# Optimization experiments

Hardware: AMD Instinct MI355X
Metric: run time of the kernel (lower is better)

## Reference

```python
import jax, jax.numpy as jnp
import numpy as np

N = 50000
E = 800000
IN_CH = 128
HID = 32
HEADS = 4
OUT_CH = 2
NEG_SLOPE = 0.2


def setup_inputs() -> dict:
    key = jax.random.key(0)
    ks = jax.random.split(key, 10)
    x = jax.random.normal(ks[0], (N, IN_CH), dtype=jnp.float32)
    edge_index = jax.random.randint(ks[1], (2, E), 0, N, dtype=jnp.int32)
    s1 = 1.0 / np.sqrt(IN_CH)
    s2 = 1.0 / np.sqrt(HEADS * HID)
    return {
        "x": x,
        "edge_index": edge_index,
        "W1": jax.random.normal(ks[2], (IN_CH, HEADS * HID), dtype=jnp.float32) * s1,
        "a_src1": jax.random.normal(ks[3], (HEADS, HID), dtype=jnp.float32) * s2,
        "a_dst1": jax.random.normal(ks[4], (HEADS, HID), dtype=jnp.float32) * s2,
        "b1": jnp.zeros((HEADS * HID,), dtype=jnp.float32),
        "W2": jax.random.normal(ks[5], (HEADS * HID, 1 * OUT_CH), dtype=jnp.float32) * s2,
        "a_src2": jax.random.normal(ks[6], (1, OUT_CH), dtype=jnp.float32),
        "a_dst2": jax.random.normal(ks[7], (1, OUT_CH), dtype=jnp.float32),
        "b2": jnp.zeros((OUT_CH,), dtype=jnp.float32),
    }


def gat_layer(x, edge_index, W, a_src, a_dst, bias, heads, out_ch, concat):
    # PyG GATConv: linear -> per-node attn terms -> per-edge LeakyReLU ->
    # softmax over incoming edges (self-loops added) -> scatter-add aggregate.
    n = x.shape[0]
    loop = jnp.arange(n, dtype=edge_index.dtype)
    src = jnp.concatenate([edge_index[0], loop])  # [E+N]
    dst = jnp.concatenate([edge_index[1], loop])
    h = (x @ W).reshape(n, heads, out_ch)                 # [N, H, C]
    a_s = jnp.einsum('nhc,hc->nh', h, a_src)              # [N, H]
    a_d = jnp.einsum('nhc,hc->nh', h, a_dst)
    e = jax.nn.leaky_relu(a_s[src] + a_d[dst], NEG_SLOPE)  # [E+N, H]
    m = jax.ops.segment_max(e, dst, num_segments=n)
    m = jax.lax.stop_gradient(jnp.where(jnp.isfinite(m), m, 0.0))
    p = jnp.exp(e - m[dst])
    denom = jax.ops.segment_sum(p, dst, num_segments=n)
    alpha = p / (denom[dst] + 1e-16)                       # softmax per dst node
    msg = h[src] * alpha[:, :, None]                       # [E+N, H, C]
    out = jax.ops.segment_sum(msg, dst, num_segments=n)    # [N, H, C]
    out = out.reshape(n, heads * out_ch) if concat else out.mean(axis=1)
    return out + bias


def reference(x, edge_index, W1, a_src1, a_dst1, b1, W2, a_src2, a_dst2, b2):
    h = gat_layer(x, edge_index, W1, a_src1, a_dst1, b1, HEADS, HID, True)
    h = jax.nn.relu(h)  # dropout is identity in eval mode
    o = gat_layer(h, edge_index, W2, a_src2, a_dst2, b2, 1, OUT_CH, False)
    return jax.nn.log_softmax(o, axis=1)
```

## Files before the change

kernel.cpp:

```cpp
#include <hip/hip_runtime.h>
#include <hip/hip_bf16.h>

#define NEG_SLOPE 0.2f
#define INV_LN2 1.44269504088896340736f
#define BSH   6
#define BUKSZ 64
#define MAXBUK 1024
#define CHUNK 2048
#define CAP   2048
#define CAPSH 11
#define XPAD  136

typedef __attribute__((ext_vector_type(8))) short bf16x8;
typedef __attribute__((ext_vector_type(4))) float f32x4;

__device__ __forceinline__ float exp2lrelu(float z) {
    return __builtin_amdgcn_exp2f(fmaxf(z, NEG_SLOPE * z));
}

__device__ __forceinline__ unsigned short f2bf(float f) {
    unsigned int u = __float_as_uint(f);
    u = (u + 0x7fffu + ((u >> 16) & 1u)) >> 16;
    return (unsigned short)u;
}

__device__ __forceinline__ float2 bfpair(unsigned int u) {
    float2 r;
    r.x = __uint_as_float(u << 16);
    r.y = __uint_as_float(u & 0xffff0000u);
    return r;
}

__global__ __launch_bounds__(256) void k0_prep(const float* __restrict__ W1,
                                               const float* __restrict__ a_src1,
                                               const float* __restrict__ a_dst1,
                                               unsigned short* __restrict__ w1t,
                                               int* __restrict__ gcur, int nbuk) {
    int g = blockIdx.x * 256 + threadIdx.x;
    if (g < nbuk) gcur[g] = 0;
    if (g < 128 * 128) {
        int k = g >> 7, nn = g & 127;
        w1t[nn * 128 + k] = f2bf(W1[g]);
    } else if (g < 128 * 128 + 1024) {
        int e = g - 128 * 128;
        int row8 = e >> 7;
        int k = e & 127;
        int h = row8 & 3;
        const float* av = (row8 < 4) ? a_src1 : a_dst1;
        float s = 0.f;
#pragma unroll
        for (int c = 0; c < 32; ++c)
            s += W1[k * 128 + h * 32 + c] * av[h * 32 + c];
        w1t[(128 + row8) * 128 + k] = f2bf(s * INV_LN2);
    } else if (g < 128 * 128 + 2048) {
        int e = g - (128 * 128 + 1024);
        w1t[(136 + (e >> 7)) * 128 + (e & 127)] = 0;
    }
}

__global__ __launch_bounds__(256) void k1_fat(const float* __restrict__ x,
                                              const unsigned short* __restrict__ w1t,
                                              unsigned short* __restrict__ h1b,
                                              float* __restrict__ a_s1,
                                              float* __restrict__ a_d1, int n,
                                              const int* __restrict__ e_src,
                                              const int* __restrict__ e_dst, int e,
                                              int nbuk, int nblk,
                                              int* __restrict__ gcur,
                                              unsigned int* __restrict__ part) {
    __shared__ unsigned short wsh[144 * XPAD];
    const int tid = threadIdx.x;

    if (blockIdx.x < (unsigned)nblk) {
        int* lcur = (int*)wsh;
        const int bid = blockIdx.x;
        const int e0 = bid * CHUNK;
        const int e1 = min(e, e0 + CHUNK);
        for (int b = tid; b < nbuk; b += 256) lcur[b] = 0;
        __syncthreads();
        for (int k = e0 + tid; k < e1; k += 256)
            atomicAdd(&lcur[e_dst[k] >> BSH], 1);
        __syncthreads();
        for (int b = tid; b < nbuk; b += 256) {
            int c = lcur[b];
            if (c) lcur[b] = (b << CAPSH) + atomicAdd(&gcur[b], c);
        }
        __syncthreads();
        for (int k = e0 + tid; k < e1; k += 256) {
            int d = e_dst[k];
            int b = d >> BSH;
            int pos = atomicAdd(&lcur[b], 1);
            if (pos < ((b + 1) << CAPSH))
                part[pos] = ((unsigned int)e_src[k] << 16) | (unsigned int)(d & 0xffff);
        }
        return;
    }

    const int row0 = (blockIdx.x - nblk) * 64;
    {
        const bf16x8* w1v = (const bf16x8*)w1t;
#pragma unroll
        for (int ii = 0; ii < 9; ++ii) {
            int i = tid + ii * 256;
            int r = i >> 4, c = (i & 15) * 8;
            *(bf16x8*)&wsh[r * XPAD + c] = w1v[i];
        }
    }

    const int wave = tid >> 6;
    const int lane = tid & 63;
    const int quad = lane >> 4;
    const int l16 = lane & 15;

    const int arow = row0 + wave * 16 + l16;
    const bool rowok = arow < n;
    const float* __restrict__ xr = x + (size_t)arow * 128;
    bf16x8 afrag[4];
#pragma unroll
    for (int ks = 0; ks < 4; ++ks) {
        float4 u = make_float4(0.f, 0.f, 0.f, 0.f), v = u;
        if (rowok) {
            u = *(const float4*)&xr[ks * 32 + quad * 8];
            v = *(const float4*)&xr[ks * 32 + quad * 8 + 4];
        }
        bf16x8 a;
        a[0] = (short)f2bf(u.x); a[1] = (short)f2bf(u.y);
        a[2] = (short)f2bf(u.z); a[3] = (short)f2bf(u.w);
        a[4] = (short)f2bf(v.x); a[5] = (short)f2bf(v.y);
        a[6] = (short)f2bf(v.z); a[7] = (short)f2bf(v.w);
        afrag[ks] = a;
    }
    __syncthreads();

    f32x4 acc[9];
#pragma unroll
    for (int t = 0; t < 9; ++t) acc[t] = (f32x4){0.f, 0.f, 0.f, 0.f};

#pragma unroll
    for (int t = 0; t < 9; ++t) {
#pragma unroll
        for (int ks = 0; ks < 4; ++ks) {
            bf16x8 bfrag = *(const bf16x8*)&wsh[(t * 16 + l16) * XPAD + ks * 32 + quad * 8];
            acc[t] = __builtin_amdgcn_mfma_f32_16x16x32_bf16(afrag[ks], bfrag, acc[t], 0, 0, 0);
        }
    }

#pragma unroll
    for (int r = 0; r < 4; ++r) {
        int gr = row0 + wave * 16 + quad * 4 + r;
        if (gr < n) {
            if (l16 < 4)      a_s1[gr * 4 + l16]       = acc[8][r];
            else if (l16 < 8) a_d1[gr * 4 + (l16 - 4)] = acc[8][r];
        }
    }

    __syncthreads();
#pragma unroll
    for (int t = 0; t < 8; ++t)
#pragma unroll
        for (int r = 0; r < 4; ++r)
            wsh[(wave * 16 + quad * 4 + r) * XPAD + t * 16 + l16] = f2bf(acc[t][r]);
    __syncthreads();
#pragma unroll
    for (int i = 0; i < 8; ++i) {
        int idx = tid + i * 256;
        int r = idx >> 5;
        int c = (idx & 31) * 4;
        int gr = row0 + r;
        if (gr < n)
            *(ushort4*)&h1b[(size_t)gr * 128 + c] = *(ushort4*)&wsh[r * XPAD + c];
    }
}

__global__ __launch_bounds__(256) void kc_csr(const unsigned int* __restrict__ part,
                                              const int* __restrict__ gcur, int nbuk,
                                              int2* __restrict__ rsd,
                                              unsigned short* __restrict__ csr_src) {
    __shared__ int cnt[64];
    __shared__ int cur[64];
    const int b = blockIdx.x;
    const int tid = threadIdx.x;
    const int eb = b << CAPSH;
    const int nE = min(gcur[b], CAP);
    if (tid < 64) cnt[tid] = 0;
    __syncthreads();
    for (int k = tid; k < nE; k += 256)
        atomicAdd(&cnt[part[eb + k] & 63u], 1);
    __syncthreads();
    if (tid < 64) {
        int v = cnt[tid];
        int incl = v;
#pragma unroll
        for (int off = 1; off < 64; off <<= 1) {
            int t = __shfl_up(incl, off);
            if (tid >= off) incl += t;
        }
        cur[tid] = incl - v;
        rsd[(b << BSH) + tid] = make_int2(eb + incl - v, v);
    }
    __syncthreads();
    for (int k = tid; k < nE; k += 256) {
        unsigned int u = part[eb + k];
        int pos = atomicAdd(&cur[u & 63u], 1);
        csr_src[eb + pos] = (unsigned short)(u >> 16);
    }
}

__global__ __launch_bounds__(256) void k3_agg1(
    const unsigned short* __restrict__ h1b, const float* __restrict__ a_s1,
    const float* __restrict__ a_d1, const int2* __restrict__ rsd,
    const unsigned short* __restrict__ csr_src, const float* __restrict__ b1,
    const float* __restrict__ W2, const float* __restrict__ a_src2,
    const float* __restrict__ a_dst2, float4* __restrict__ pk, int n) {
    const int wid = (blockIdx.x * blockDim.x + threadIdx.x) >> 6;
    const int lane = threadIdx.x & 63;
    if (wid >= n) return;
    const int q = lane >> 4;
    const int l16 = lane & 15;
    const int c0 = l16 * 8;
    const unsigned cb = (unsigned)l16 * 16u;
    const int head = l16 >> 2;
    const int2 rd = rsd[wid];
    const int rs = rd.x;
    const int deg = rd.y;
    const float ad = a_d1[wid * 4 + head];
    const char* __restrict__ h1c = (const char*)h1b;
    const unsigned short* __restrict__ crs = csr_src + rs;

    float dnm = 0.f;
    float acc[8] = {};
    const int nfull = deg >> 4;
    const int dm1 = deg - 1;
    int j = q;
    for (int it = 0; it < nfull; ++it, j += 16) {
        unsigned s0 = (unsigned)crs[j];
        unsigned s1 = (unsigned)crs[j + 4];
        unsigned s2 = (unsigned)crs[j + 8];
        unsigned s3 = (unsigned)crs[j + 12];
        float as0 = a_s1[(s0 << 2) + head];
        float as1 = a_s1[(s1 << 2) + head];
        float as2 = a_s1[(s2 << 2) + head];
        float as3 = a_s1[(s3 << 2) + head];
        uint4 g0 = *(const uint4*)(h1c + ((s0 << 8) + cb));
        uint4 g1 = *(const uint4*)(h1c + ((s1 << 8) + cb));
        uint4 g2 = *(const uint4*)(h1c + ((s2 << 8) + cb));
        uint4 g3 = *(const uint4*)(h1c + ((s3 << 8) + cb));
        float p0 = exp2lrelu(as0 + ad);
        float p1 = exp2lrelu(as1 + ad);
        float p2 = exp2lrelu(as2 + ad);
        float p3 = exp2lrelu(as3 + ad);
        dnm += (p0 + p1) + (p2 + p3);
        float2 v0a = bfpair(g0.x), v0b = bfpair(g0.y), v0c = bfpair(g0.z), v0d = bfpair(g0.w);
        float2 v1a = bfpair(g1.x), v1b = bfpair(g1.y), v1c = bfpair(g1.z), v1d = bfpair(g1.w);
        float2 v2a = bfpair(g2.x), v2b = bfpair(g2.y), v2c = bfpair(g2.z), v2d = bfpair(g2.w);
        float2 v3a = bfpair(g3.x), v3b = bfpair(g3.y), v3c = bfpair(g3.z), v3d = bfpair(g3.w);
        acc[0] += (p0 * v0a.x + p1 * v1a.x) + (p2 * v2a.x + p3 * v3a.x);
        acc[1] += (p0 * v0a.y + p1 * v1a.y) + (p2 * v2a.y + p3 * v3a.y);
        acc[2] += (p0 * v0b.x + p1 * v1b.x) + (p2 * v2b.x + p3 * v3b.x);
        acc[3] += (p0 * v0b.y + p1 * v1b.y) + (p2 * v2b.y + p3 * v3b.y);
        acc[4] += (p0 * v0c.x + p1 * v1c.x) + (p2 * v2c.x + p3 * v3c.x);
        acc[5] += (p0 * v0c.y + p1 * v1c.y) + (p2 * v2c.y + p3 * v3c.y);
        acc[6] += (p0 * v0d.x + p1 * v1d.x) + (p2 * v2d.x + p3 * v3d.x);
        acc[7] += (p0 * v0d.y + p1 * v1d.y) + (p2 * v2d.y + p3 * v3d.y);
    }
    for (int t = nfull << 4; t < deg; t += 4) {
        const int slot = t + q;
        const bool b0 = slot < deg;
        unsigned s0 = (unsigned)crs[min(slot, dm1)];
        float as0 = a_s1[(s0 << 2) + head];
        uint4 g0 = make_uint4(0, 0, 0, 0);
        if (b0) g0 = *(const uint4*)(h1c + ((s0 << 8) + cb));
        float p0 = b0 ? exp2lrelu(as0 + ad) : 0.f;
        dnm += p0;
        float2 va = bfpair(g0.x), vb = bfpair(g0.y), vc = bfpair(g0.z), vd = bfpair(g0.w);
        acc[0] += p0 * va.x;  acc[1] += p0 * va.y;
        acc[2] += p0 * vb.x;  acc[3] += p0 * vb.y;
        acc[4] += p0 * vc.x;  acc[5] += p0 * vc.y;
        acc[6] += p0 * vd.x;  acc[7] += p0 * vd.y;
    }
    dnm += __shfl_xor(dnm, 16);
    dnm += __shfl_xor(dnm, 32);
#pragma unroll
    for (int k = 0; k < 8; ++k) {
        acc[k] += __shfl_xor(acc[k], 16);
        acc[k] += __shfl_xor(acc[k], 32);
    }
    {
        float p = exp2lrelu(a_s1[wid * 4 + head] + ad);
        uint4 gs = *(const uint4*)(h1c + (((unsigned)wid << 8) + cb));
        float2 ha = bfpair(gs.x), hb = bfpair(gs.y), hc = bfpair(gs.z), hd2 = bfpair(gs.w);
        dnm += p;
        acc[0] += p * ha.x;  acc[1] += p * ha.y;
        acc[2] += p * hb.x;  acc[3] += p * hb.y;
        acc[4] += p * hc.x;  acc[5] += p * hc.y;
        acc[6] += p * hd2.x; acc[7] += p * hd2.y;
    }
    float inv = 1.f / (dnm + 1e-16f);
    float r[8];
    float4 bva = *(const float4*)&b1[c0];
    float4 bvb = *(const float4*)&b1[c0 + 4];
    r[0] = fmaxf(acc[0] * inv + bva.x, 0.f);
    r[1] = fmaxf(acc[1] * inv + bva.y, 0.f);
    r[2] = fmaxf(acc[2] * inv + bva.z, 0.f);
    r[3] = fmaxf(acc[3] * inv + bva.w, 0.f);
    r[4] = fmaxf(acc[4] * inv + bvb.x, 0.f);
    r[5] = fmaxf(acc[5] * inv + bvb.y, 0.f);
    r[6] = fmaxf(acc[6] * inv + bvb.z, 0.f);
    r[7] = fmaxf(acc[7] * inv + bvb.w, 0.f);

    float p0 = 0.f, p1 = 0.f;
#pragma unroll
    for (int k = 0; k < 4; ++k) {
        float4 w = *(const float4*)&W2[c0 * 2 + k * 4];
        p0 += r[2 * k] * w.x + r[2 * k + 1] * w.z;
        p1 += r[2 * k] * w.y + r[2 * k + 1] * w.w;
    }
#pragma unroll
    for (int off = 1; off < 16; off <<= 1) {
        p0 += __shfl_xor(p0, off);
        p1 += __shfl_xor(p1, off);
    }
    if (lane == 0) {
        pk[wid] = make_float4(p0, p1,
                              (p0 * a_src2[0] + p1 * a_src2[1]) * INV_LN2,
                              (p0 * a_dst2[0] + p1 * a_dst2[1]) * INV_LN2);
    }
}

__global__ __launch_bounds__(256) void k4_agg2(
    const float4* __restrict__ pk, const int2* __restrict__ rsd,
    const unsigned short* __restrict__ csr_src, const float* __restrict__ b2,
    float* __restrict__ out, int n) {
    const int g = blockIdx.x * blockDim.x + threadIdx.x;
    const int lane = threadIdx.x & 63;
    const int node = (g >> 6) * 4 + (lane >> 4);
    const int l16 = lane & 15;
    if (node >= n) return;
    const int2 rd = rsd[node];
    const int rs = rd.x;
    const int deg = rd.y;
    const float4 me = pk[node];
    const float ad = me.w;

    float dnm = 0.f, a0 = 0.f, a1 = 0.f;
    for (int j = l16; j < deg; j += 16) {
        int s = (int)csr_src[rs + j];
        float4 qv = pk[s];
        float p = exp2lrelu(qv.z + ad);
        dnm += p;
        a0 += p * qv.x;
        a1 += p * qv.y;
    }
    if (l16 == 0) {
        float p = exp2lrelu(me.z + ad);
        dnm += p;
        a0 += p * me.x;
        a1 += p * me.y;
    }
#pragma unroll
    for (int off = 1; off < 16; off <<= 1) {
        dnm += __shfl_xor(dnm, off);
        a0 += __shfl_xor(a0, off);
        a1 += __shfl_xor(a1, off);
    }
    if (l16 == 0) {
        float inv = 1.f / (dnm + 1e-16f);
        float o0 = a0 * inv + b2[0];
        float o1 = a1 * inv + b2[1];
        float m2 = fmaxf(o0, o1);
        float lse = m2 + logf(__expf(o0 - m2) + __expf(o1 - m2));
        out[node * 2 + 0] = o0 - lse;
        out[node * 2 + 1] = o1 - lse;
    }
}

extern "C" void kernel_launch(void* const* d_in, const int* in_sizes, int n_in,
                              void* d_out, int out_size, void* d_ws, size_t ws_size,
                              hipStream_t stream) {
    const float* x      = (const float*)d_in[0];
    const int*   ei     = (const int*)d_in[1];
    const float* W1     = (const float*)d_in[2];
    const float* a_src1 = (const float*)d_in[3];
    const float* a_dst1 = (const float*)d_in[4];
    const float* b1     = (const float*)d_in[5];
    const float* W2     = (const float*)d_in[6];
    const float* a_src2 = (const float*)d_in[7];
    const float* a_dst2 = (const float*)d_in[8];
    const float* b2     = (const float*)d_in[9];
    float* out = (float*)d_out;

    const int N = in_sizes[0] / 128;
    const int E = in_sizes[1] / 2;
    const int* e_src = ei;
    const int* e_dst = ei + E;

    const int NBUK = (N + BUKSZ - 1) >> BSH;
    const int nblk = (E + CHUNK - 1) / CHUNK;
    const int gemmBlocks = (N + 63) / 64;

    char* p = (char*)d_ws;
    auto alloc = [&](size_t bytes) -> void* {
        void* r = (void*)p;
        p += (bytes + 255) & ~(size_t)255;
        return r;
    };
    unsigned short* h1b   = (unsigned short*)alloc((size_t)N * 128 * 2);
    float*          a_s1  = (float*)alloc((size_t)N * 4 * 4);
    float*          a_d1  = (float*)alloc((size_t)N * 4 * 4);
    float4*         pk    = (float4*)alloc((size_t)N * 16);
    unsigned short* w1t   = (unsigned short*)alloc((size_t)144 * 128 * 2);
    int*            gcur  = (int*)alloc((size_t)NBUK * 4);
    unsigned int*   part  = (unsigned int*)alloc((size_t)NBUK * CAP * 4);
    int2*           rsd   = (int2*)alloc((size_t)(NBUK << BSH) * 8);
    unsigned short* csr_src = (unsigned short*)alloc((size_t)NBUK * CAP * 2);

    k0_prep<<<72, 256, 0, stream>>>(W1, a_src1, a_dst1, w1t, gcur, NBUK);
    k1_fat<<<nblk + gemmBlocks, 256, 0, stream>>>(x, w1t, h1b, a_s1, a_d1, N,
                                                  e_src, e_dst, E, NBUK, nblk,
                                                  gcur, part);
    kc_csr<<<NBUK, 256, 0, stream>>>(part, gcur, NBUK, rsd, csr_src);
    k3_agg1<<<(N * 64 + 255) / 256, 256, 0, stream>>>(h1b, a_s1, a_d1, rsd, csr_src,
                                                      b1, W2, a_src2, a_dst2, pk, N);
    k4_agg2<<<((N + 3) / 4 * 64 + 255) / 256, 256, 0, stream>>>(pk, rsd, csr_src,
                                                                b2, out, N);
}
```

Before: 162.8 us.

## Fuse per-bucket CSR construction into layer-1 aggregation kernel using shared memory

Merges the bucket-local CSR build and the layer-1 aggregation into one kernel of 512 threads per 64-node bucket. Source indices are sorted into an LDS array and read from there during aggregation, while still being written to global memory for the layer-2 kernel. This removes one launch and the global round trip of the CSR for layer 1. In exchange each wave now handles 8 nodes one after another, and the grid shrinks to about 782 blocks, which reduces parallelism and latency hiding for the gathers.

```diff
diff --git a/kernel.cpp b/kernel.cpp
--- a/kernel.cpp
+++ b/kernel.cpp
@@ -172,19 +172,25 @@
     }
 }
 
-__global__ __launch_bounds__(256) void kc_csr(const unsigned int* __restrict__ part,
-                                              const int* __restrict__ gcur, int nbuk,
-                                              int2* __restrict__ rsd,
-                                              unsigned short* __restrict__ csr_src) {
+__global__ __launch_bounds__(512) void k3_agg1(
+    const unsigned int* __restrict__ part, const int* __restrict__ gcur,
+    const unsigned short* __restrict__ h1b, const float* __restrict__ a_s1,
+    const float* __restrict__ a_d1, const float* __restrict__ b1,
+    const float* __restrict__ W2, const float* __restrict__ a_src2,
+    const float* __restrict__ a_dst2, float4* __restrict__ pk,
+    int2* __restrict__ rsd, unsigned short* __restrict__ csr_src, int n) {
+    __shared__ unsigned short lcsr[CAP];
     __shared__ int cnt[64];
     __shared__ int cur[64];
+    __shared__ int lst[64];
     const int b = blockIdx.x;
     const int tid = threadIdx.x;
     const int eb = b << CAPSH;
     const int nE = min(gcur[b], CAP);
+
     if (tid < 64) cnt[tid] = 0;
     __syncthreads();
-    for (int k = tid; k < nE; k += 256)
+    for (int k = tid; k < nE; k += 512)
         atomicAdd(&cnt[part[eb + k] & 63u], 1);
     __syncthreads();
     if (tid < 64) {
@@ -195,135 +201,136 @@
             int t = __shfl_up(incl, off);
             if (tid >= off) incl += t;
         }
-        cur[tid] = incl - v;
-        rsd[(b << BSH) + tid] = make_int2(eb + incl - v, v);
-    }
-    __syncthreads();
-    for (int k = tid; k < nE; k += 256) {
+        int excl = incl - v;
+        lst[tid] = excl;
+        cur[tid] = excl;
+        rsd[(b << BSH) + tid] = make_int2(eb + excl, v);
+    }
+    __syncthreads();
+    for (int k = tid; k < nE; k += 512) {
         unsigned int u = part[eb + k];
         int pos = atomicAdd(&cur[u & 63u], 1);
-        csr_src[eb + pos] = (unsigned short)(u >> 16);
-    }
-}
-
-__global__ __launch_bounds__(256) void k3_agg1(
-    const unsigned short* __restrict__ h1b, const float* __restrict__ a_s1,
-    const float* __restrict__ a_d1, const int2* __restrict__ rsd,
-    const unsigned short* __restrict__ csr_src, const float* __restrict__ b1,
-    const float* __restrict__ W2, const float* __restrict__ a_src2,
-    const float* __restrict__ a_dst2, float4* __restrict__ pk, int n) {
-    const int wid = (blockIdx.x * blockDim.x + threadIdx.x) >> 6;
-    const int lane = threadIdx.x & 63;
-    if (wid >= n) return;
+        lcsr[pos] = (unsigned short)(u >> 16);
+    }
+    __syncthreads();
+    for (int k = tid; k < nE; k += 512)
+        csr_src[eb + k] = lcsr[k];
+
+    const int wv = tid >> 6;
+    const int lane = tid & 63;
     const int q = lane >> 4;
     const int l16 = lane & 15;
     const int c0 = l16 * 8;
     const unsigned cb = (unsigned)l16 * 16u;
     const int head = l16 >> 2;
-    const int2 rd = rsd[wid];
-    const int rs = rd.x;
-    const int deg = rd.y;
-    const float ad = a_d1[wid * 4 + head];
     const char* __restrict__ h1c = (const char*)h1b;
-    const unsigned short* __restrict__ crs = csr_src + rs;
-
-    float dnm = 0.f;
-    float acc[8] = {};
-    const int nfull = deg >> 4;
-    const int dm1 = deg - 1;
-    int j = q;
-    for (int it = 0; it < nfull; ++it, j += 16) {
-        unsigned s0 = (unsigned)crs[j];
-        unsigned s1 = (unsigned)crs[j + 4];
-        unsigned s2 = (unsigned)crs[j + 8];
-        unsigned s3 = (unsigned)crs[j + 12];
-        float as0 = a_s1[(s0 << 2) + head];
-        float as1 = a_s1[(s1 << 2) + head];
-        float as2 = a_s1[(s2 << 2) + head];
-        float as3 = a_s1[(s3 << 2) + head];
-        uint4 g0 = *(const uint4*)(h1c + ((s0 << 8) + cb));
-        uint4 g1 = *(const uint4*)(h1c + ((s1 << 8) + cb));
-        uint4 g2 = *(const uint4*)(h1c + ((s2 << 8) + cb));
-        uint4 g3 = *(const uint4*)(h1c + ((s3 << 8) + cb));
-        float p0 = exp2lrelu(as0 + ad);
-        float p1 = exp2lrelu(as1 + ad);
-        float p2 = exp2lrelu(as2 + ad);
-        float p3 = exp2lrelu(as3 + ad);
-        dnm += (p0 + p1) + (p2 + p3);
-        float2 v0a = bfpair(g0.x), v0b = bfpair(g0.y), v0c = bfpair(g0.z), v0d = bfpair(g0.w);
-        float2 v1a = bfpair(g1.x), v1b = bfpair(g1.y), v1c = bfpair(g1.z), v1d = bfpair(g1.w);
-        float2 v2a = bfpair(g2.x), v2b = bfpair(g2.y), v2c = bfpair(g2.z), v2d = bfpair(g2.w);
-        float2 v3a = bfpair(g3.x), v3b = bfpair(g3.y), v3c = bfpair(g3.z), v3d = bfpair(g3.w);
-        acc[0] += (p0 * v0a.x + p1 * v1a.x) + (p2 * v2a.x + p3 * v3a.x);
-        acc[1] += (p0 * v0a.y + p1 * v1a.y) + (p2 * v2a.y + p3 * v3a.y);
-        acc[2] += (p0 * v0b.x + p1 * v1b.x) + (p2 * v2b.x + p3 * v3b.x);
-        acc[3] += (p0 * v0b.y + p1 * v1b.y) + (p2 * v2b.y + p3 * v3b.y);
-        acc[4] += (p0 * v0c.x + p1 * v1c.x) + (p2 * v2c.x + p3 * v3c.x);
-        acc[5] += (p0 * v0c.y + p1 * v1c.y) + (p2 * v2c.y + p3 * v3c.y);
-        acc[6] += (p0 * v0d.x + p1 * v1d.x) + (p2 * v2d.x + p3 * v3d.x);
-        acc[7] += (p0 * v0d.y + p1 * v1d.y) + (p2 * v2d.y + p3 * v3d.y);
-    }
-    for (int t = nfull << 4; t < deg; t += 4) {
-        const int slot = t + q;
-        const bool b0 = slot < deg;
-        unsigned s0 = (unsigned)crs[min(slot, dm1)];
-        float as0 = a_s1[(s0 << 2) + head];
-        uint4 g0 = make_uint4(0, 0, 0, 0);
-        if (b0) g0 = *(const uint4*)(h1c + ((s0 << 8) + cb));
-        float p0 = b0 ? exp2lrelu(as0 + ad) : 0.f;
-        dnm += p0;
-        float2 va = bfpair(g0.x), vb = bfpair(g0.y), vc = bfpair(g0.z), vd = bfpair(g0.w);
-        acc[0] += p0 * va.x;  acc[1] += p0 * va.y;
-        acc[2] += p0 * vb.x;  acc[3] += p0 * vb.y;
-        acc[4] += p0 * vc.x;  acc[5] += p0 * vc.y;
-        acc[6] += p0 * vd.x;  acc[7] += p0 * vd.y;
-    }
-    dnm += __shfl_xor(dnm, 16);
-    dnm += __shfl_xor(dnm, 32);
-#pragma unroll
-    for (int k = 0; k < 8; ++k) {
-        acc[k] += __shfl_xor(acc[k], 16);
-        acc[k] += __shfl_xor(acc[k], 32);
-    }
-    {
-        float p = exp2lrelu(a_s1[wid * 4 + head] + ad);
-        uint4 gs = *(const uint4*)(h1c + (((unsigned)wid << 8) + cb));
-        float2 ha = bfpair(gs.x), hb = bfpair(gs.y), hc = bfpair(gs.z), hd2 = bfpair(gs.w);
-        dnm += p;
-        acc[0] += p * ha.x;  acc[1] += p * ha.y;
-        acc[2] += p * hb.x;  acc[3] += p * hb.y;
-        acc[4] += p * hc.x;  acc[5] += p * hc.y;
-        acc[6] += p * hd2.x; acc[7] += p * hd2.y;
-    }
-    float inv = 1.f / (dnm + 1e-16f);
-    float r[8];
-    float4 bva = *(const float4*)&b1[c0];
-    float4 bvb = *(const float4*)&b1[c0 + 4];
-    r[0] = fmaxf(acc[0] * inv + bva.x, 0.f);
-    r[1] = fmaxf(acc[1] * inv + bva.y, 0.f);
-    r[2] = fmaxf(acc[2] * inv + bva.z, 0.f);
-    r[3] = fmaxf(acc[3] * inv + bva.w, 0.f);
-    r[4] = fmaxf(acc[4] * inv + bvb.x, 0.f);
-    r[5] = fmaxf(acc[5] * inv + bvb.y, 0.f);
-    r[6] = fmaxf(acc[6] * inv + bvb.z, 0.f);
-    r[7] = fmaxf(acc[7] * inv + bvb.w, 0.f);
-
-    float p0 = 0.f, p1 = 0.f;
-#pragma unroll
-    for (int k = 0; k < 4; ++k) {
-        float4 w = *(const float4*)&W2[c0 * 2 + k * 4];
-        p0 += r[2 * k] * w.x + r[2 * k + 1] * w.z;
-        p1 += r[2 * k] * w.y + r[2 * k + 1] * w.w;
-    }
-#pragma unroll
-    for (int off = 1; off < 16; off <<= 1) {
-        p0 += __shfl_xor(p0, off);
-        p1 += __shfl_xor(p1, off);
-    }
-    if (lane == 0) {
-        pk[wid] = make_float4(p0, p1,
-                              (p0 * a_src2[0] + p1 * a_src2[1]) * INV_LN2,
-                              (p0 * a_dst2[0] + p1 * a_dst2[1]) * INV_LN2);
+
+    for (int i = 0; i < 8; ++i) {
+        const int node = (b << BSH) + (wv << 3) + i;
+        if (node >= n) continue;
+        const int nl = node & 63;
+        const int ls = lst[nl];
+        const int deg = cnt[nl];
+        const float ad = a_d1[node * 4 + head];
+
+        float dnm = 0.f;
+        float acc[8] = {};
+        const int nfull = deg >> 4;
+        const int dm1 = deg - 1;
+        int j = q;
+        for (int it = 0; it < nfull; ++it, j += 16) {
+            unsigned s0 = (unsigned)lcsr[ls + j];
+            unsigned s1 = (unsigned)lcsr[ls + j + 4];
+            unsigned s2 = (unsigned)lcsr[ls + j + 8];
+            unsigned s3 = (unsigned)lcsr[ls + j + 12];
+            float as0 = a_s1[(s0 << 2) + head];
+            float as1 = a_s1[(s1 << 2) + head];
+            float as2 = a_s1[(s2 << 2) + head];
+            float as3 = a_s1[(s3 << 2) + head];
+            uint4 g0 = *(const uint4*)(h1c + ((s0 << 8) + cb));
+            uint4 g1 = *(const uint4*)(h1c + ((s1 << 8) + cb));
+            uint4 g2 = *(const uint4*)(h1c + ((s2 << 8) + cb));
+            uint4 g3 = *(const uint4*)(h1c + ((s3 << 8) + cb));
+            float p0 = exp2lrelu(as0 + ad);
+            float p1 = exp2lrelu(as1 + ad);
+            float p2 = exp2lrelu(as2 + ad);
+            float p3 = exp2lrelu(as3 + ad);
+            dnm += (p0 + p1) + (p2 + p3);
+            float2 v0a = bfpair(g0.x), v0b = bfpair(g0.y), v0c = bfpair(g0.z), v0d = bfpair(g0.w);
+            float2 v1a = bfpair(g1.x), v1b = bfpair(g1.y), v1c = bfpair(g1.z), v1d = bfpair(g1.w);
+            float2 v2a = bfpair(g2.x), v2b = bfpair(g2.y), v2c = bfpair(g2.z), v2d = bfpair(g2.w);
+            float2 v3a = bfpair(g3.x), v3b = bfpair(g3.y), v3c = bfpair(g3.z), v3d = bfpair(g3.w);
+            acc[0] += (p0 * v0a.x + p1 * v1a.x) + (p2 * v2a.x + p3 * v3a.x);
+            acc[1] += (p0 * v0a.y + p1 * v1a.y) + (p2 * v2a.y + p3 * v3a.y);
+            acc[2] += (p0 * v0b.x + p1 * v1b.x) + (p2 * v2b.x + p3 * v3b.x);
+            acc[3] += (p0 * v0b.y + p1 * v1b.y) + (p2 * v2b.y + p3 * v3b.y);
+            acc[4] += (p0 * v0c.x + p1 * v1c.x) + (p2 * v2c.x + p3 * v3c.x);
+            acc[5] += (p0 * v0c.y + p1 * v1c.y) + (p2 * v2c.y + p3 * v3c.y);
+            acc[6] += (p0 * v0d.x + p1 * v1d.x) + (p2 * v2d.x + p3 * v3d.x);
+            acc[7] += (p0 * v0d.y + p1 * v1d.y) + (p2 * v2d.y + p3 * v3d.y);
+        }
+        for (int t = nfull << 4; t < deg; t += 4) {
+            const int slot = t + q;
+            const bool ok = slot < deg;
+            unsigned s0 = (unsigned)lcsr[ls + min(slot, dm1)];
+            float as0 = a_s1[(s0 << 2) + head];
+            uint4 g0 = make_uint4(0, 0, 0, 0);
+            if (ok) g0 = *(const uint4*)(h1c + ((s0 << 8) + cb));
+            float p0 = ok ? exp2lrelu(as0 + ad) : 0.f;
+            dnm += p0;
+            float2 va = bfpair(g0.x), vb = bfpair(g0.y), vc = bfpair(g0.z), vd = bfpair(g0.w);
+            acc[0] += p0 * va.x;  acc[1] += p0 * va.y;
+            acc[2] += p0 * vb.x;  acc[3] += p0 * vb.y;
+            acc[4] += p0 * vc.x;  acc[5] += p0 * vc.y;
+            acc[6] += p0 * vd.x;  acc[7] += p0 * vd.y;
+        }
+        dnm += __shfl_xor(dnm, 16);
+        dnm += __shfl_xor(dnm, 32);
+#pragma unroll
+        for (int k = 0; k < 8; ++k) {
+            acc[k] += __shfl_xor(acc[k], 16);
+            acc[k] += __shfl_xor(acc[k], 32);
+        }
+        {
+            float p = exp2lrelu(a_s1[node * 4 + head] + ad);
+            uint4 gs = *(const uint4*)(h1c + (((unsigned)node << 8) + cb));
+            float2 ha = bfpair(gs.x), hb = bfpair(gs.y), hc = bfpair(gs.z), hd2 = bfpair(gs.w);
+            dnm += p;
+            acc[0] += p * ha.x;  acc[1] += p * ha.y;
+            acc[2] += p * hb.x;  acc[3] += p * hb.y;
+            acc[4] += p * hc.x;  acc[5] += p * hc.y;
+            acc[6] += p * hd2.x; acc[7] += p * hd2.y;
+        }
+        float inv = 1.f / (dnm + 1e-16f);
+        float r[8];
+        float4 bva = *(const float4*)&b1[c0];
+        float4 bvb = *(const float4*)&b1[c0 + 4];
+        r[0] = fmaxf(acc[0] * inv + bva.x, 0.f);
+        r[1] = fmaxf(acc[1] * inv + bva.y, 0.f);
+        r[2] = fmaxf(acc[2] * inv + bva.z, 0.f);
+        r[3] = fmaxf(acc[3] * inv + bva.w, 0.f);
+        r[4] = fmaxf(acc[4] * inv + bvb.x, 0.f);
+        r[5] = fmaxf(acc[5] * inv + bvb.y, 0.f);
+        r[6] = fmaxf(acc[6] * inv + bvb.z, 0.f);
+        r[7] = fmaxf(acc[7] * inv + bvb.w, 0.f);
+
+        float p0 = 0.f, p1 = 0.f;
+#pragma unroll
+        for (int k = 0; k < 4; ++k) {
+            float4 w = *(const float4*)&W2[c0 * 2 + k * 4];
+            p0 += r[2 * k] * w.x + r[2 * k + 1] * w.z;
+            p1 += r[2 * k] * w.y + r[2 * k + 1] * w.w;
+        }
+#pragma unroll
+        for (int off = 1; off < 16; off <<= 1) {
+            p0 += __shfl_xor(p0, off);
+            p1 += __shfl_xor(p1, off);
+        }
+        if (lane == 0) {
+            pk[node] = make_float4(p0, p1,
+                                   (p0 * a_src2[0] + p1 * a_src2[1]) * INV_LN2,
+                                   (p0 * a_dst2[0] + p1 * a_dst2[1]) * INV_LN2);
+        }
     }
 }
 
@@ -418,9 +425,8 @@
     k1_fat<<<nblk + gemmBlocks, 256, 0, stream>>>(x, w1t, h1b, a_s1, a_d1, N,
                                                   e_src, e_dst, E, NBUK, nblk,
                                                   gcur, part);
-    kc_csr<<<NBUK, 256, 0, stream>>>(part, gcur, NBUK, rsd, csr_src);
-    k3_agg1<<<(N * 64 + 255) / 256, 256, 0, stream>>>(h1b, a_s1, a_d1, rsd, csr_src,
-                                                      b1, W2, a_src2, a_dst2, pk, N);
+    k3_agg1<<<NBUK, 512, 0, stream>>>(part, gcur, h1b, a_s1, a_d1,
+                                      b1, W2, a_src2, a_dst2, pk, rsd, csr_src, N);
     k4_agg2<<<((N + 3) / 4 * 64 + 255) / 256, 256, 0, stream>>>(pk, rsd, csr_src,
                                                                 b2, out, N);
 }
```

Measured after the change: 163.8 us, median of 2. No clear change (+0.6%).
